# Kernel tuning notes

Measured on AMD Instinct MI355X. Metric: run time of the kernel, lower is better.

The kernel has to match this reference:

```python
import jax, jax.numpy as jnp
import numpy as np

N = 100000
E = 640000
ND = 128   # node_dim
ED = 128   # edge_dim
HD = 256   # hidden_dim
EPS = 1e-5


def _mlp_ln(x, W1, b1, W2, b2, W3, b3, g, beta):
    h = jax.nn.relu(x @ W1 + b1)
    h = jax.nn.relu(h @ W2 + b2)
    o = h @ W3 + b3
    mu = jnp.mean(o, axis=-1, keepdims=True)
    var = jnp.mean(jnp.square(o - mu), axis=-1, keepdims=True)
    return (o - mu) * jax.lax.rsqrt(var + EPS) * g + beta


def setup_inputs() -> dict:
    key = jax.random.key(0)
    ks = jax.random.split(key, 20)
    s = 0.02
    inp = {
        "node_emb": jax.random.normal(ks[0], (N, ND), jnp.float32),
        "edge_emb": jax.random.normal(ks[1], (E, ED), jnp.float32),
        "src": jax.random.randint(ks[2], (E,), 0, N),
        "dst": jax.random.randint(ks[3], (E,), 0, N),
        "num_nodes": N,
        # edge MLP: in = 2*ND + ED
        "eW1": jax.random.normal(ks[4], (2 * ND + ED, HD), jnp.float32) * s,
        "eb1": jnp.zeros((HD,), jnp.float32),
        "eW2": jax.random.normal(ks[5], (HD, HD), jnp.float32) * s,
        "eb2": jnp.zeros((HD,), jnp.float32),
        "eW3": jax.random.normal(ks[6], (HD, ED), jnp.float32) * s,
        "eb3": jnp.zeros((ED,), jnp.float32),
        "eg": jnp.ones((ED,), jnp.float32),
        "ebeta": jnp.zeros((ED,), jnp.float32),
        # node MLP: in = ND + ED
        "nW1": jax.random.normal(ks[7], (ND + ED, HD), jnp.float32) * s,
        "nb1": jnp.zeros((HD,), jnp.float32),
        "nW2": jax.random.normal(ks[8], (HD, HD), jnp.float32) * s,
        "nb2": jnp.zeros((HD,), jnp.float32),
        "nW3": jax.random.normal(ks[9], (HD, ND), jnp.float32) * s,
        "nb3": jnp.zeros((ND,), jnp.float32),
        "ng": jnp.ones((ND,), jnp.float32),
        "nbeta": jnp.zeros((ND,), jnp.float32),
    }
    return inp


def reference(node_emb, edge_emb, src, dst, num_nodes,
              eW1, eb1, eW2, eb2, eW3, eb3, eg, ebeta,
              nW1, nb1, nW2, nb2, nW3, nb3, ng, nbeta):
    # Edge update: e' = MLP(concat(h_i, h_j, e)) + e
    edge_input = jnp.concatenate([node_emb[src], node_emb[dst], edge_emb], axis=-1)
    edge_emb_new = _mlp_ln(edge_input, eW1, eb1, eW2, eb2, eW3, eb3, eg, ebeta) + edge_emb
    # Mean aggregation over incoming edges per dst node
    agg = jax.ops.segment_sum(edge_emb_new, dst, num_segments=num_nodes)
    count = jax.ops.segment_sum(jnp.ones((dst.shape[0], 1), node_emb.dtype), dst, num_segments=num_nodes)
    agg = agg / jnp.maximum(count, 1.0)
    # Node update: h' = MLP(concat(h, agg)) + h
    node_input = jnp.concatenate([node_emb, agg], axis=-1)
    node_emb_new = _mlp_ln(node_input, nW1, nb1, nW2, nb2, nW3, nb3, ng, nbeta) + node_emb
    return (node_emb_new, edge_emb_new)
```

## Files before the change

### kernel.cpp

```cpp
#include <hip/hip_runtime.h>
#include <hip/hip_bf16.h>

typedef __attribute__((ext_vector_type(8))) short bf16x8;
typedef __attribute__((ext_vector_type(4))) short s16x4;
typedef __attribute__((ext_vector_type(4))) float f32x4;

__device__ __forceinline__ short f2bf(float f) {
  union { __hip_bfloat16 h; short s; } u;
  u.h = __float2bfloat16(f);
  return u.s;
}

__device__ __forceinline__ void gld_lds16(const short* g, short* l) {
  __builtin_amdgcn_global_load_lds((const __attribute__((address_space(1))) unsigned*)g,
                                   (__attribute__((address_space(3))) unsigned*)l,
                                   16, 0, 0);
}

#define BARX(N) asm volatile("s_waitcnt vmcnt(" #N ") lgkmcnt(0)\ns_barrier" ::: "memory")
#define BARLG() asm volatile("s_waitcnt lgkmcnt(0)\ns_barrier" ::: "memory")

__global__ void cvt_count_kernel(const float* __restrict__ in, short* __restrict__ out, long n8,
                                 const int* __restrict__ dst, int* __restrict__ cnt, int E) {
  const long T = (long)gridDim.x * blockDim.x;
  const long t0 = (long)blockIdx.x * blockDim.x + threadIdx.x;
  for (long i = t0; i < n8; i += T) {
    const float* p = in + i * 8;
    float4 a = *(const float4*)p, b = *(const float4*)(p + 4);
    bf16x8 o;
    o[0] = f2bf(a.x); o[1] = f2bf(a.y); o[2] = f2bf(a.z); o[3] = f2bf(a.w);
    o[4] = f2bf(b.x); o[5] = f2bf(b.y); o[6] = f2bf(b.z); o[7] = f2bf(b.w);
    *(bf16x8*)(out + i * 8) = o;
  }
  for (long j = t0; j < E; j += T) atomicAdd(&cnt[dst[j]], 1);
}

__global__ void prep_all_kernel(const float* __restrict__ eW1, const float* __restrict__ eW2,
                                const float* __restrict__ eW3, const float* __restrict__ nW1,
                                const float* __restrict__ nW2, const float* __restrict__ nW3,
                                short* __restrict__ eAll, short* __restrict__ nAll) {
  int b = blockIdx.x;
  const float* W; short* out; int K, N; bool perm;
  if (b < 48)       { W = eW1; out = eAll;          K = 384; N = 256; perm = false; }
  else if (b < 80)  { W = eW2; out = eAll + 98304;  K = 256; N = 256; perm = true;  b -= 48; }
  else if (b < 96)  { W = eW3; out = eAll + 163840; K = 256; N = 128; perm = true;  b -= 80; }
  else if (b < 128) { W = nW1; out = nAll;          K = 256; N = 256; perm = false; b -= 96; }
  else if (b < 160) { W = nW2; out = nAll + 65536;  K = 256; N = 256; perm = true;  b -= 128; }
  else              { W = nW3; out = nAll + 131072; K = 256; N = 128; perm = true;  b -= 160; }
  int s = b * 256 + threadIdx.x;
  int NF = N >> 4;
  int total = (K >> 5) * NF * 64;
  if (s >= total) return;
  int l = s & 63, kcf = s >> 6;
  int kc = kcf / NF, f = kcf - kc * NF;
  int kg = l >> 4, l16 = l & 15;
  bf16x8 o;
#pragma unroll
  for (int e = 0; e < 8; ++e) {
    int kh = kc * 32 + kg * 8 + e;
    int k = perm ? ((kh & ~63) | ((kh & 3) << 4) | ((kh >> 2) & 15)) : kh;
    o[e] = f2bf(W[(size_t)k * N + f * 16 + l16]);
  }
  *(bf16x8*)(out + (size_t)s * 8) = o;
}

__global__ void bsum_kernel(const int* __restrict__ cnt, int* __restrict__ bsum, int N) {
  __shared__ int wsum[4];
  int b = blockIdx.x, t = threadIdx.x;
  int base = b * 2048;
  int s = 0;
#pragma unroll
  for (int j = 0; j < 8; ++j) {
    int i = base + j * 256 + t;
    s += (i < N) ? cnt[i] : 0;
  }
#pragma unroll
  for (int m = 1; m < 64; m <<= 1) s += __shfl_xor(s, m);
  if ((t & 63) == 0) wsum[t >> 6] = s;
  __syncthreads();
  if (t == 0) bsum[b] = wsum[0] + wsum[1] + wsum[2] + wsum[3];
}

__global__ void bscan_kernel(int* __restrict__ bsum, int nb) {
  int l = threadIdx.x;
  int v = (l < nb) ? bsum[l] : 0;
  int x = v;
#pragma unroll
  for (int d = 1; d < 64; d <<= 1) { int y = __shfl_up(x, d); if (l >= d) x += y; }
  if (l < nb) bsum[l] = x - v;
}

__global__ void offs_kernel(const int* __restrict__ cnt, const int* __restrict__ bsum,
                            int* __restrict__ off, int* __restrict__ cursor, int N) {
  __shared__ int wpre[4];
  int b = blockIdx.x, t = threadIdx.x, w = t >> 6, l = t & 63;
  int base = b * 2048;
  int v[8];
  int s = 0;
#pragma unroll
  for (int j = 0; j < 8; ++j) {
    int i = base + t * 8 + j;
    v[j] = (i < N) ? cnt[i] : 0;
    s += v[j];
  }
  int x = s;
#pragma unroll
  for (int d = 1; d < 64; d <<= 1) { int y = __shfl_up(x, d); if (l >= d) x += y; }
  if (l == 63) wpre[w] = x;
  __syncthreads();
  int wo = 0;
  for (int k = 0; k < w; ++k) wo += wpre[k];
  int excl = bsum[b] + wo + x - s;
#pragma unroll
  for (int j = 0; j < 8; ++j) {
    int i = base + t * 8 + j;
    if (i < N) { off[i] = excl; cursor[i] = excl; }
    excl += v[j];
  }
  if (b == gridDim.x - 1 && t == 255) off[N] = excl;
}

__global__ void scatter_kernel(const int* __restrict__ dst, int* __restrict__ cursor,
                               int* __restrict__ eidx, int E) {
  int e = blockIdx.x * 256 + threadIdx.x;
  if (e < E) {
    int p = atomicAdd(&cursor[dst[e]], 1);
    eidx[p] = e;
  }
}

__global__ void agg_kernel(const float* __restrict__ edge_out, const int* __restrict__ eidx,
                           const int* __restrict__ off, short* __restrict__ aggb, int N) {
  int n = blockIdx.x * 4 + (threadIdx.x >> 6);
  if (n >= N) return;
  int l = threadIdx.x & 63;
  int beg = off[n], end = off[n + 1];
  float ax = 0.f, ay = 0.f;
  int i = beg;
  for (; i + 4 <= end; i += 4) {
    int e0 = eidx[i], e1 = eidx[i + 1], e2 = eidx[i + 2], e3 = eidx[i + 3];
    float2 v0 = *(const float2*)(edge_out + (size_t)e0 * 128 + l * 2);
    float2 v1 = *(const float2*)(edge_out + (size_t)e1 * 128 + l * 2);
    float2 v2 = *(const float2*)(edge_out + (size_t)e2 * 128 + l * 2);
    float2 v3 = *(const float2*)(edge_out + (size_t)e3 * 128 + l * 2);
    ax += v0.x + v1.x + v2.x + v3.x;
    ay += v0.y + v1.y + v2.y + v3.y;
  }
  for (; i < end; ++i) {
    int e = eidx[i];
    float2 v = *(const float2*)(edge_out + (size_t)e * 128 + l * 2);
    ax += v.x; ay += v.y;
  }
  float inv = 1.0f / fmaxf((float)(end - beg), 1.0f);
  unsigned pk = ((unsigned)(unsigned short)f2bf(ay * inv) << 16) |
                (unsigned)(unsigned short)f2bf(ax * inv);
  *(unsigned*)&aggb[(size_t)n * 128 + l * 2] = pk;
}

struct F8 { float4 a, b; };

template <bool IS_EDGE>
__launch_bounds__(512)
__global__ void mlp_kernel(const float* __restrict__ node_emb_f, const float* __restrict__ edge_emb_f,
                           const short* __restrict__ node_bf, const short* __restrict__ agg_bf,
                           const int* __restrict__ src, const int* __restrict__ dst,
                           const short* __restrict__ wAll,
                           const float* __restrict__ b1, const float* __restrict__ b2,
                           const float* __restrict__ b3,
                           const float* __restrict__ gam, const float* __restrict__ bet,
                           float* __restrict__ out_base, int M) {
  extern __shared__ short smem[];
  short* Bs = smem;
  short* Hs = smem + 24576;

  const int tid = threadIdx.x;
  const int m0 = blockIdx.x * 128;
  const int w = tid >> 6, lane = tid & 63, l16 = lane & 15, kg = lane >> 4;
  const int wr = w >> 2, wc = w & 3;

  constexpr int NL1 = IS_EDGE ? 12 : 8;

  const int grow = ((tid >> 6) & 7) * 16 + (tid & 15);
  const int gcq = ((tid >> 4) & 3) * 8;
  const int grc = min(m0 + grow, M - 1);
  int gsr = 0, gdr = 0;
  if (IS_EDGE) { gsr = src[grc]; gdr = dst[grc]; }

  float b1v[4], b2v[4];
#pragma unroll
  for (int ct = 0; ct < 4; ++ct) {
    int col = wc * 64 + ct * 16 + l16;
    b1v[ct] = b1[col];
    b2v[ct] = b2[col];
  }
  float b3v[8], gv[8], bev[8];
#pragma unroll
  for (int f = 0; f < 8; ++f) {
    int col = f * 16 + l16;
    b3v[f] = b3[col]; gv[f] = gam[col]; bev[f] = bet[col];
  }

  f32x4 acc[16];
#pragma unroll
  for (int i = 0; i < 16; ++i) { f32x4 z = {0.f, 0.f, 0.f, 0.f}; acc[i] = z; }

  auto stageW = [&](int v) {
    const short* g = wAll + (size_t)v * 8192;
    short* l = Bs + (size_t)(v % 3) * 8192;
    gld_lds16(g + (size_t)tid * 8, l + (size_t)tid * 8);
    gld_lds16(g + (size_t)(tid + 512) * 8, l + (size_t)(tid + 512) * 8);
  };
  auto stageAb = [&](int v) {
    short* dstp = Hs + (size_t)(v % 3) * 4096 + (size_t)tid * 8;
    int col = v * 32 + gcq;
    const short* q;
    if (IS_EDGE) {
      q = node_bf + (size_t)(col < 128 ? gsr : gdr) * 128 + (col & 127);
    } else {
      q = (col < 128) ? node_bf + (size_t)grc * 128 + col
                      : agg_bf + (size_t)grc * 128 + (col - 128);
    }
    gld_lds16(q, dstp);
  };
  auto loadAf = [&](int v) -> F8 {
    const float* q = edge_emb_f + (size_t)grc * 128 + (v * 32 + gcq - 256);
    F8 r;
    r.a = *(const float4*)q;
    r.b = *(const float4*)(q + 4);
    return r;
  };
  auto storeAf = [&](int v, const F8& p) {
    float t[8];
    *(float4*)t = p.a; *(float4*)(t + 4) = p.b;
    bf16x8 o;
#pragma unroll
    for (int e = 0; e < 8; ++e) o[e] = f2bf(t[e]);
    *(bf16x8*)(Hs + (size_t)(v % 3) * 4096 + (size_t)tid * 8) = o;
  };

  auto compA = [&](int u) {
    const short* Ap = Hs + (size_t)(u % 3) * 4096;
    const short* Bp = Bs + (size_t)(u % 3) * 8192;
    bf16x8 a[4], b[4];
#pragma unroll
    for (int rt = 0; rt < 4; ++rt)
      a[rt] = *(const bf16x8*)&Ap[(size_t)((wr * 4 + rt) * 64 + lane) * 8];
#pragma unroll
    for (int ct = 0; ct < 4; ++ct)
      b[ct] = *(const bf16x8*)&Bp[(size_t)((wc * 4 + ct) * 64 + lane) * 8];
#pragma unroll
    for (int rt = 0; rt < 4; ++rt)
#pragma unroll
      for (int ct = 0; ct < 4; ++ct)
        acc[rt * 4 + ct] = __builtin_amdgcn_mfma_f32_16x16x32_bf16(a[rt], b[ct], acc[rt * 4 + ct], 0, 0, 0);
  };

  auto compH = [&](int kc, const short* Bp) {
    bf16x8 a[4], b[4];
#pragma unroll
    for (int rt = 0; rt < 4; ++rt) {
      int row = wr * 64 + rt * 16 + l16;
      int ch = (kc * 32 + kg * 8) ^ ((row & 7) << 3);
      a[rt] = *(const bf16x8*)&Hs[(size_t)row * 256 + ch];
    }
#pragma unroll
    for (int ct = 0; ct < 4; ++ct)
      b[ct] = *(const bf16x8*)&Bp[(size_t)((wc * 4 + ct) * 64 + lane) * 8];
#pragma unroll
    for (int rt = 0; rt < 4; ++rt)
#pragma unroll
      for (int ct = 0; ct < 4; ++ct)
        acc[rt * 4 + ct] = __builtin_amdgcn_mfma_f32_16x16x32_bf16(a[rt], b[ct], acc[rt * 4 + ct], 0, 0, 0);
  };

  auto writeH = [&](const float* bv) {
#pragma unroll
    for (int rt = 0; rt < 4; ++rt)
#pragma unroll
      for (int q = 0; q < 4; ++q) {
        int row = wr * 64 + rt * 16 + kg * 4 + q;
        s16x4 v;
#pragma unroll
        for (int ct = 0; ct < 4; ++ct)
          v[ct] = f2bf(fmaxf(acc[rt * 4 + ct][q] + bv[ct], 0.f));
        int ch = (wc * 64 + l16 * 4) ^ ((row & 7) << 3);
        *(s16x4*)&Hs[(size_t)row * 256 + ch] = v;
      }
#pragma unroll
    for (int i = 0; i < 16; ++i) { f32x4 z = {0.f, 0.f, 0.f, 0.f}; acc[i] = z; }
  };

  auto compL3 = [&](int kk, const short* Bp) {
    int row = w * 16 + l16;
    int ch = (kk * 32 + kg * 8) ^ ((row & 7) << 3);
    bf16x8 a = *(const bf16x8*)&Hs[(size_t)row * 256 + ch];
    const short* Bsub = Bp + (size_t)(kk & 1) * 4096;
#pragma unroll
    for (int f = 0; f < 8; ++f) {
      bf16x8 b = *(const bf16x8*)&Bsub[(size_t)(f * 64 + lane) * 8];
      acc[f] = __builtin_amdgcn_mfma_f32_16x16x32_bf16(a, b, acc[f], 0, 0, 0);
    }
  };

  stageW(0);
  stageAb(0);
  stageW(1);
  stageAb(1);
  BARX(3);

#pragma unroll 1
  for (int u = 0; u < 6; ++u) {
    stageW(u + 2);
    stageAb(u + 2);
    compA(u);
    BARX(3);
  }

  if (IS_EDGE) {
#pragma unroll 1
    for (int u = 6; u < 10; ++u) {
      F8 p = loadAf(u + 2);
      stageW(u + 2);
      compA(u);
      storeAf(u + 2, p);
      BARX(2);
    }
  }

#pragma unroll 1
  for (int u = NL1 - 2; u < NL1; ++u) {
    stageW(u + 2);
    compA(u);
    BARX(2);
  }
  writeH(b1v);
  BARLG();

#pragma unroll 1
  for (int u = NL1; u < NL1 + 8; ++u) {
    stageW(u + 2);
    compH(u - NL1, Bs + (size_t)(u % 3) * 8192);
    BARX(2);
  }
  writeH(b2v);
  BARLG();

  {
    const int us = NL1 + 8;
#pragma unroll 1
    for (int k = 0; k < 2; ++k) {
      int u = us + k;
      stageW(u + 2);
      const short* Bp = Bs + (size_t)(u % 3) * 8192;
      compL3(2 * k, Bp);
      compL3(2 * k + 1, Bp);
      BARX(2);
    }
    {
      const short* Bp = Bs + (size_t)((us + 2) % 3) * 8192;
      compL3(4, Bp);
      compL3(5, Bp);
      BARX(0);
    }
    {
      const short* Bp = Bs + (size_t)((us + 3) % 3) * 8192;
      compL3(6, Bp);
      compL3(7, Bp);
    }
  }

#pragma unroll
  for (int q = 0; q < 4; ++q) {
    int rg = m0 + w * 16 + kg * 4 + q;
    float o[8], s1 = 0.f, s2 = 0.f;
#pragma unroll
    for (int f = 0; f < 8; ++f) {
      float x = acc[f][q] + b3v[f];
      o[f] = x; s1 += x; s2 += x * x;
    }
#pragma unroll
    for (int m = 1; m <= 8; m <<= 1) { s1 += __shfl_xor(s1, m); s2 += __shfl_xor(s2, m); }
    float mu = s1 * (1.f / 128.f);
    float var = s2 * (1.f / 128.f) - mu * mu;
    float rs = rsqrtf(var + 1e-5f);
    if (rg < M) {
      const float* resid = (IS_EDGE ? edge_emb_f : node_emb_f) + (size_t)rg * 128;
      float* op = out_base + (size_t)rg * 128;
#pragma unroll
      for (int f = 0; f < 8; ++f) {
        int col = f * 16 + l16;
        op[col] = (o[f] - mu) * rs * gv[f] + bev[f] + resid[col];
      }
    }
  }
}

extern "C" void kernel_launch(void* const* d_in, const int* in_sizes, int n_in,
                              void* d_out, int out_size, void* d_ws, size_t ws_size,
                              hipStream_t stream) {
  const float* node_emb = (const float*)d_in[0];
  const float* edge_emb = (const float*)d_in[1];
  const int*   src      = (const int*)d_in[2];
  const int*   dst      = (const int*)d_in[3];
  const float* eW1 = (const float*)d_in[5];
  const float* eb1 = (const float*)d_in[6];
  const float* eW2 = (const float*)d_in[7];
  const float* eb2 = (const float*)d_in[8];
  const float* eW3 = (const float*)d_in[9];
  const float* eb3 = (const float*)d_in[10];
  const float* eg  = (const float*)d_in[11];
  const float* ebt = (const float*)d_in[12];
  const float* nW1 = (const float*)d_in[13];
  const float* nb1 = (const float*)d_in[14];
  const float* nW2 = (const float*)d_in[15];
  const float* nb2 = (const float*)d_in[16];
  const float* nW3 = (const float*)d_in[17];
  const float* nb3 = (const float*)d_in[18];
  const float* ng  = (const float*)d_in[19];
  const float* nbt = (const float*)d_in[20];

  const int Nn = in_sizes[0] / 128;
  const int Ee = in_sizes[2];
  const int nb2048 = (Nn + 2047) / 2048;

  char* ws = (char*)d_ws;
  short* aggb   = (short*)ws;  ws += (size_t)Nn * 128 * 2;
  short* nodebf = (short*)ws;  ws += (size_t)Nn * 128 * 2;
  int* cnt_i  = (int*)ws;      ws += (size_t)Nn * 4;
  int* cursor = (int*)ws;      ws += (size_t)Nn * 4;
  int* offv   = (int*)ws;      ws += (size_t)(Nn + 1) * 4;
  int* eidx   = (int*)ws;      ws += (size_t)Ee * 4;
  int* bsum   = (int*)ws;      ws += 64 * 4;
  ws = (char*)(((uintptr_t)ws + 15) & ~(uintptr_t)15);
  short* eAll = (short*)ws;
  short* nAll = eAll + 196608;

  float* out_node = (float*)d_out;
  float* out_edge = out_node + (size_t)Nn * 128;

  hipMemsetAsync(cnt_i, 0, (size_t)Nn * 4, stream);

  cvt_count_kernel<<<2048, 256, 0, stream>>>(node_emb, nodebf, (long)Nn * 16, dst, cnt_i, Ee);
  prep_all_kernel<<<176, 256, 0, stream>>>(eW1, eW2, eW3, nW1, nW2, nW3, eAll, nAll);

  bsum_kernel<<<nb2048, 256, 0, stream>>>(cnt_i, bsum, Nn);
  bscan_kernel<<<1, 64, 0, stream>>>(bsum, nb2048);
  offs_kernel<<<nb2048, 256, 0, stream>>>(cnt_i, bsum, offv, cursor, Nn);
  scatter_kernel<<<(Ee + 255) / 256, 256, 0, stream>>>(dst, cursor, eidx, Ee);

  mlp_kernel<true><<<(Ee + 127) / 128, 512, 114688, stream>>>(
      node_emb, edge_emb, nodebf, aggb, src, dst, eAll,
      eb1, eb2, eb3, eg, ebt, out_edge, Ee);

  agg_kernel<<<(Nn + 3) / 4, 256, 0, stream>>>(out_edge, eidx, offv, aggb, Nn);

  mlp_kernel<false><<<(Nn + 127) / 128, 512, 114688, stream>>>(
      node_emb, edge_emb, nodebf, aggb, src, dst, nAll,
      nb1, nb2, nb3, ng, nbt, out_node, Nn);
}
```

Before: 654.2 us.

## Deepen LDS staging to four buffers and prefetch fragments for half the waves

The kernel goes from a 3-deep to a 4-deep LDS ring for weight and activation tiles, so global-to-LDS loads are issued three stages ahead instead of two. Waves in the first row group now double-buffer their MFMA operands in registers: they read the next stage's LDS fragments right after issuing the current MFMAs, to overlap LDS latency with matrix work. Dynamic shared memory grows from 112 KB to 128 KB per block, and the prefetch raises register pressure for those waves. The aim is to hide memory latency, at the cost of more LDS use and a more complex schedule.

```diff
diff --git a/kernel.cpp b/kernel.cpp
--- a/kernel.cpp
+++ b/kernel.cpp
@@ -171,12 +171,13 @@
                            float* __restrict__ out_base, int M) {
   extern __shared__ short smem[];
   short* Bs = smem;
-  short* Hs = smem + 24576;
+  short* Hs = smem + 32768;
 
   const int tid = threadIdx.x;
   const int m0 = blockIdx.x * 128;
   const int w = tid >> 6, lane = tid & 63, l16 = lane & 15, kg = lane >> 4;
   const int wr = w >> 2, wc = w & 3;
+  const bool gA = (wr == 0);
 
   constexpr int NL1 = IS_EDGE ? 12 : 8;
 
@@ -206,12 +207,12 @@
 
   auto stageW = [&](int v) {
     const short* g = wAll + (size_t)v * 8192;
-    short* l = Bs + (size_t)(v % 3) * 8192;
+    short* l = Bs + (size_t)(v & 3) * 8192;
     gld_lds16(g + (size_t)tid * 8, l + (size_t)tid * 8);
     gld_lds16(g + (size_t)(tid + 512) * 8, l + (size_t)(tid + 512) * 8);
   };
   auto stageAb = [&](int v) {
-    short* dstp = Hs + (size_t)(v % 3) * 4096 + (size_t)tid * 8;
+    short* dstp = Hs + (size_t)(v & 3) * 4096 + (size_t)tid * 8;
     int col = v * 32 + gcq;
     const short* q;
     if (IS_EDGE) {
@@ -235,28 +236,28 @@
     bf16x8 o;
 #pragma unroll
     for (int e = 0; e < 8; ++e) o[e] = f2bf(t[e]);
-    *(bf16x8*)(Hs + (size_t)(v % 3) * 4096 + (size_t)tid * 8) = o;
-  };
-
-  auto compA = [&](int u) {
-    const short* Ap = Hs + (size_t)(u % 3) * 4096;
-    const short* Bp = Bs + (size_t)(u % 3) * 8192;
-    bf16x8 a[4], b[4];
+    *(bf16x8*)(Hs + (size_t)(v & 3) * 4096 + (size_t)tid * 8) = o;
+  };
+
+  auto mfma16v = [&](bf16x8* a, bf16x8* b) {
+#pragma unroll
+    for (int rt = 0; rt < 4; ++rt)
+#pragma unroll
+      for (int ct = 0; ct < 4; ++ct)
+        acc[rt * 4 + ct] = __builtin_amdgcn_mfma_f32_16x16x32_bf16(a[rt], b[ct], acc[rt * 4 + ct], 0, 0, 0);
+  };
+  auto readL1 = [&](int u, bf16x8* a, bf16x8* b) {
+    const short* Ap = Hs + (size_t)(u & 3) * 4096;
+    const short* Bp = Bs + (size_t)(u & 3) * 8192;
 #pragma unroll
     for (int rt = 0; rt < 4; ++rt)
       a[rt] = *(const bf16x8*)&Ap[(size_t)((wr * 4 + rt) * 64 + lane) * 8];
 #pragma unroll
     for (int ct = 0; ct < 4; ++ct)
       b[ct] = *(const bf16x8*)&Bp[(size_t)((wc * 4 + ct) * 64 + lane) * 8];
-#pragma unroll
-    for (int rt = 0; rt < 4; ++rt)
-#pragma unroll
-      for (int ct = 0; ct < 4; ++ct)
-        acc[rt * 4 + ct] = __builtin_amdgcn_mfma_f32_16x16x32_bf16(a[rt], b[ct], acc[rt * 4 + ct], 0, 0, 0);
-  };
-
-  auto compH = [&](int kc, const short* Bp) {
-    bf16x8 a[4], b[4];
+  };
+  auto readL2 = [&](int kc, int u, bf16x8* a, bf16x8* b) {
+    const short* Bp = Bs + (size_t)(u & 3) * 8192;
 #pragma unroll
     for (int rt = 0; rt < 4; ++rt) {
       int row = wr * 64 + rt * 16 + l16;
@@ -266,11 +267,31 @@
 #pragma unroll
     for (int ct = 0; ct < 4; ++ct)
       b[ct] = *(const bf16x8*)&Bp[(size_t)((wc * 4 + ct) * 64 + lane) * 8];
-#pragma unroll
-    for (int rt = 0; rt < 4; ++rt)
-#pragma unroll
-      for (int ct = 0; ct < 4; ++ct)
-        acc[rt * 4 + ct] = __builtin_amdgcn_mfma_f32_16x16x32_bf16(a[rt], b[ct], acc[rt * 4 + ct], 0, 0, 0);
+  };
+
+  bf16x8 ha[4], hb[4];
+
+  auto l1body = [&](int u, bool first, bool last) {
+    if (gA) {
+      if (first) readL1(u, ha, hb);
+      mfma16v(ha, hb);
+      if (!last) readL1(u + 1, ha, hb);
+    } else {
+      bf16x8 a[4], b[4];
+      readL1(u, a, b);
+      mfma16v(a, b);
+    }
+  };
+  auto l2body = [&](int kc, int u, bool first, bool last) {
+    if (gA) {
+      if (first) readL2(kc, u, ha, hb);
+      mfma16v(ha, hb);
+      if (!last) readL2(kc + 1, u + 1, ha, hb);
+    } else {
+      bf16x8 a[4], b[4];
+      readL2(kc, u, a, b);
+      mfma16v(a, b);
+    }
   };
 
   auto writeH = [&](const float* bv) {
@@ -302,44 +323,49 @@
     }
   };
 
-  stageW(0);
-  stageAb(0);
-  stageW(1);
-  stageAb(1);
+  stageW(0); stageAb(0);
+  stageW(1); stageAb(1);
+  stageW(2); stageAb(2);
   BARX(3);
 
 #pragma unroll 1
-  for (int u = 0; u < 6; ++u) {
-    stageW(u + 2);
-    stageAb(u + 2);
-    compA(u);
+  for (int u = 0; u < 5; ++u) {
+    stageW(u + 3);
+    stageAb(u + 3);
+    l1body(u, u == 0, false);
     BARX(3);
   }
 
   if (IS_EDGE) {
 #pragma unroll 1
-    for (int u = 6; u < 10; ++u) {
-      F8 p = loadAf(u + 2);
-      stageW(u + 2);
-      compA(u);
-      storeAf(u + 2, p);
+    for (int u = 5; u < 9; ++u) {
+      F8 p = loadAf(u + 3);
+      stageW(u + 3);
+      l1body(u, false, false);
+      storeAf(u + 3, p);
       BARX(2);
     }
-  }
-
 #pragma unroll 1
-  for (int u = NL1 - 2; u < NL1; ++u) {
-    stageW(u + 2);
-    compA(u);
-    BARX(2);
+    for (int u = 9; u < 12; ++u) {
+      stageW(u + 3);
+      l1body(u, false, u == 11);
+      BARX(2);
+    }
+  } else {
+#pragma unroll 1
+    for (int u = 5; u < 8; ++u) {
+      stageW(u + 3);
+      l1body(u, false, u == 7);
+      BARX(2);
+    }
   }
   writeH(b1v);
   BARLG();
 
 #pragma unroll 1
   for (int u = NL1; u < NL1 + 8; ++u) {
-    stageW(u + 2);
-    compH(u - NL1, Bs + (size_t)(u % 3) * 8192);
+    stageW(u + 3);
+    l2body(u - NL1, u, u == NL1, u == NL1 + 7);
     BARX(2);
   }
   writeH(b2v);
@@ -347,23 +373,27 @@
 
   {
     const int us = NL1 + 8;
-#pragma unroll 1
-    for (int k = 0; k < 2; ++k) {
-      int u = us + k;
-      stageW(u + 2);
-      const short* Bp = Bs + (size_t)(u % 3) * 8192;
-      compL3(2 * k, Bp);
-      compL3(2 * k + 1, Bp);
-      BARX(2);
-    }
+    stageW(us + 3);
     {
-      const short* Bp = Bs + (size_t)((us + 2) % 3) * 8192;
+      const short* Bp = Bs + (size_t)(us & 3) * 8192;
+      compL3(0, Bp);
+      compL3(1, Bp);
+    }
+    BARX(2);
+    {
+      const short* Bp = Bs + (size_t)((us + 1) & 3) * 8192;
+      compL3(2, Bp);
+      compL3(3, Bp);
+    }
+    BARX(2);
+    {
+      const short* Bp = Bs + (size_t)((us + 2) & 3) * 8192;
       compL3(4, Bp);
       compL3(5, Bp);
-      BARX(0);
-    }
+    }
+    BARX(0);
     {
-      const short* Bp = Bs + (size_t)((us + 3) % 3) * 8192;
+      const short* Bp = Bs + (size_t)((us + 3) & 3) * 8192;
       compL3(6, Bp);
       compL3(7, Bp);
     }
@@ -448,13 +478,13 @@
   offs_kernel<<<nb2048, 256, 0, stream>>>(cnt_i, bsum, offv, cursor, Nn);
   scatter_kernel<<<(Ee + 255) / 256, 256, 0, stream>>>(dst, cursor, eidx, Ee);
 
-  mlp_kernel<true><<<(Ee + 127) / 128, 512, 114688, stream>>>(
+  mlp_kernel<true><<<(Ee + 127) / 128, 512, 131072, stream>>>(
       node_emb, edge_emb, nodebf, aggb, src, dst, eAll,
       eb1, eb2, eb3, eg, ebt, out_edge, Ee);
 
   agg_kernel<<<(Nn + 3) / 4, 256, 0, stream>>>(out_edge, eidx, offv, aggb, Nn);
 
-  mlp_kernel<false><<<(Nn + 127) / 128, 512, 114688, stream>>>(
+  mlp_kernel<false><<<(Nn + 127) / 128, 512, 131072, stream>>>(
       node_emb, edge_emb, nodebf, aggb, src, dst, nAll,
       nb1, nb2, nb3, ng, nbt, out_node, Nn);
 }
```

Result: slower. 668.7 us (+2.2%).
